# Performance work log

Measured on AMD Instinct MI355X. Metric: run time of the kernel, lower is better.

The kernel has to match this reference:

```python
import jax, jax.numpy as jnp
import numpy as np

WINDOW = 32


def _dilate(mask, iters=5):
    # scipy binary_dilation with default cross structure, `iters` iterations
    m = mask.copy()
    for _ in range(iters):
        d = m.copy()
        d[1:, :] |= m[:-1, :]
        d[:-1, :] |= m[1:, :]
        d[:, 1:] |= m[:, :-1]
        d[:, :-1] |= m[:, 1:]
        m = d
    return m


def _label8(mask):
    # skimage measure.label, default 8-connectivity, via min-label propagation
    h, w = mask.shape
    lab = np.where(mask, np.arange(1, mask.size + 1, dtype=np.int64).reshape(h, w), 0)
    BIG = mask.size + 2
    while True:
        p = np.pad(np.where(mask, lab, BIG), 1, constant_values=BIG)
        m = np.full((h, w), BIG, dtype=np.int64)
        for dy in (-1, 0, 1):
            for dx in (-1, 0, 1):
                m = np.minimum(m, p[1 + dy:1 + dy + h, 1 + dx:1 + dx + w])
        new = np.where(mask, m, 0)
        if np.array_equal(new, lab):
            break
        lab = new
    u = np.unique(lab)
    out = np.searchsorted(u, lab)
    if u[0] != 0:
        out = out + 1
    return out


def _malis(seg_flat, e1, e2, costs, pos):
    # MALIS edge weights: Kruskal on descending affinities with union-find;
    # pos=True counts same-(nonzero)-label pairs merged by each edge,
    # pos=False counts cross-label pairs between labeled nodes.
    n = seg_flat.size
    parent = np.arange(n)
    cnt = [dict() for _ in range(n)]
    for i in range(n):
        s = int(seg_flat[i])
        if s != 0:
            cnt[i][s] = 1
    w = np.zeros(costs.shape[0], np.float32)

    def find(x):
        r = x
        while parent[r] != r:
            r = parent[r]
        while parent[x] != r:
            parent[x], x = r, parent[x]
        return r

    order = np.argsort(-costs, kind='stable')
    for ei in order:
        ra, rb = find(int(e1[ei])), find(int(e2[ei]))
        if ra == rb:
            continue
        ca, cb = cnt[ra], cnt[rb]
        small, large = (ca, cb) if len(ca) <= len(cb) else (cb, ca)
        same = 0
        for kk, v in small.items():
            same += v * large.get(kk, 0)
        if pos:
            w[ei] = same
        else:
            sa = sum(ca.values())
            sb = sum(cb.values())
            w[ei] = sa * sb - same
        parent[rb] = ra
        for kk, v in cb.items():
            ca[kk] = ca.get(kk, 0) + v
        cnt[rb] = None
    return w


def compute_malis_weights(pred_np, target_np):
    B, C, H, W = pred_np.shape
    wn_full = np.zeros(pred_np.shape, np.float32)
    wp_full = np.zeros(pred_np.shape, np.float32)
    win = WINDOW
    idx = np.arange(win * win).reshape(win, win)
    e1 = np.concatenate([idx[:, :-1].ravel(), idx[:-1, :].ravel()])
    e2 = np.concatenate([idx[:, 1:].ravel(), idx[1:, :].ravel()])
    for k in range(H // win):
        for j in range(W // win):
            p = pred_np[:, :, k * win:(k + 1) * win, j * win:(j + 1) * win]
            t = target_np[:, :, k * win:(k + 1) * win, j * win:(j + 1) * win]
            costs = np.concatenate([
                (p[:, :, :, :-1] + p[:, :, :, 1:]).reshape(B, -1),
                (p[:, :, :-1, :] + p[:, :, 1:, :]).reshape(B, -1)], axis=1).astype(np.float32)
            gtc = np.concatenate([
                (t[:, :, :, :-1] + t[:, :, :, 1:]).reshape(B, -1),
                (t[:, :, :-1, :] + t[:, :, 1:, :]).reshape(B, -1)], axis=1).astype(np.float32)
            costs_n = costs.copy()
            costs_p = costs.copy()
            costs_n[gtc > 20] = 20
            costs_p[gtc < 10] = 0
            gtc = np.minimum(gtc, 20)
            for i in range(B):
                sg = _label8(_dilate(t[i, 0] == 0, 5) == 0)
                en = _malis(sg.ravel(), e1, e2, costs_n[i], False)
                ep = _malis(sg.ravel(), e1, e2, costs_p[i], True)
                sn = en.sum()
                if sn > 0:
                    en = en / sn
                sp = ep.sum()
                if sp > 0:
                    ep = ep / sp
                en[gtc[i] >= 10] = 0
                ep[gtc[i] < 20] = 0
                for ew, out in ((en, wn_full), (ep, wp_full)):
                    wh, wv = np.split(ew, 2)
                    wh = wh.reshape(win, win - 1)
                    wv = wv.reshape(win - 1, win)
                    nodes = np.zeros((win, win), np.float32)
                    nodes[:, :-1] += wh
                    nodes[:, 1:] += wh
                    nodes[:-1, :] += wv
                    nodes[1:, :] += wv
                    out[i, 0, k * win:(k + 1) * win, j * win:(j + 1) * win] = nodes
    return wn_full, wp_full


def setup_inputs() -> dict:
    key = jax.random.key(0)
    k1, k2 = jax.random.split(key)
    pred = jax.random.uniform(k1, (2, 1, 256, 256), jnp.float32) * 20.0
    target = jax.random.randint(k2, (2, 1, 256, 256), 0, 26).astype(jnp.float32)
    return {"pred": pred, "target": target, "malis_lr": 1.0, "malis_lr_pos": 1.0}


def reference(pred, target, malis_lr, malis_lr_pos):
    # weights are computed from detached values (CPU graph algorithm), constants wrt autodiff
    wn, wp = compute_malis_weights(np.asarray(pred), np.asarray(target))
    wn = jnp.asarray(wn, jnp.float32)
    wp = jnp.asarray(wp, jnp.float32)
    loss = malis_lr * jnp.square(pred) * wn + malis_lr_pos * jnp.square(20.0 - pred) * wp
    return loss.sum()
```

## Files before the change

### kernel.cpp

```cpp
#include <hip/hip_runtime.h>
#include <cstdint>

#define NPIX  1024
#define NH    992
#define NEDGE 1984
#define NSORT 2048
#define NGRP  31
#define HFS   4300
#define POOLN (NPIX + 2*HFS)

typedef unsigned long long u64;
typedef unsigned int u32;

static __device__ __forceinline__ u64 packRoot(int sL,int off,int len,int cap){
    return (u64)(u32)(sL & 0x7FF) | ((u64)(u32)(off & 0x3FFF) << 11) |
           ((u64)(u32)(len & 0x7FF) << 25) | ((u64)(u32)(cap & 0x7FF) << 36);
}
#define R_SL(R)  ((int)((R) & 0x7FF))
#define R_OFF(R) ((int)(((R)>>11) & 0x3FFF))
#define R_LEN(R) ((int)(((R)>>25) & 0x7FF))
#define R_CAP(R) ((int)(((R)>>36) & 0x7FF))

static __device__ __forceinline__ int rdl(int v, int l){ return __builtin_amdgcn_readlane(v, l); }

static __device__ __forceinline__ u64 sxor64(u64 v, int m){
    u32 lo = (u32)__shfl_xor((int)(v & 0xFFFFFFFFull), m, 64);
    u32 hi = (u32)__shfl_xor((int)(v >> 32), m, 64);
    return ((u64)hi << 32) | lo;
}

#define CE(x, y, up) { u64 _a=(x), _b=(y); bool _lt=(_a<_b); \
    u64 _mn=_lt?_a:_b, _mx=_lt?_b:_a; (x)=(up)?_mn:_mx; (y)=(up)?_mx:_mn; }
#define CEX(x, xm, keepmin) { u64 _p=sxor64((x),(xm)); bool _lt=((x)<_p); \
    u64 _mn=_lt?(x):_p, _mx=_lt?_p:(x); (x)=(keepmin)?_mn:_mx; }

static __device__ __forceinline__ int wredi(int v){
    #pragma unroll
    for (int o = 32; o > 0; o >>= 1) v += __shfl_xor(v, o, 64);
    return v;
}
static __device__ __forceinline__ float wredf(float v){
    #pragma unroll
    for (int o = 32; o > 0; o >>= 1) v += __shfl_xor(v, o, 64);
    return v;
}

__global__ __launch_bounds__(128) void malis_kernel(
    const float* __restrict__ pred,
    const float* __restrict__ target,
    const float* __restrict__ lr_p,
    const float* __restrict__ lrp_p,
    float* __restrict__ out)
{
    const int tid  = threadIdx.x;
    const int lane = tid & 63;
    const int wv   = tid >> 6;
    const int bid  = blockIdx.x;
    const int bb   = bid >> 6;
    const int win  = bid & 63;
    const int wy   = win >> 3, wx = win & 7;
    const int base = bb * 65536 + (wy * 32) * 256 + wx * 32;

    __shared__ __align__(16) u32 Ks[2][NSORT];
    __shared__ u64   root[2][NPIX];
    __shared__ float predL[NPIX];
    __shared__ float costs[NEDGE];
    __shared__ u32   eab[NEDGE];
    __shared__ u32   poolS[2][POOLN];
    __shared__ u32   Q[2][NPIX];
    __shared__ float Qw[2][NPIX];
    __shared__ short seg[NPIX];
    __shared__ short par[2][NPIX];
    __shared__ short H[2][NPIX + 1];
    __shared__ unsigned char tgtL[NPIX];
    __shared__ unsigned char gtcL[NEDGE];
    __shared__ int   flags[2];

    unsigned char* mA    = (unsigned char*)poolS;
    unsigned char* mB    = mA + NPIX;
    short*         labId = (short*)(mA + 2 * NPIX);

    for (int i = tid; i < NPIX; i += 128) {
        int r = i >> 5, c = i & 31;
        float pv = pred[base + r * 256 + c];
        float tv = target[base + r * 256 + c];
        predL[i] = pv;
        tgtL[i]  = (unsigned char)tv;
        mA[i]    = (tv == 0.0f) ? 1 : 0;
    }
    if (tid == 0) flags[1] = 0;
    __syncthreads();

    unsigned char* srcm = mA;
    unsigned char* dstm = mB;
    for (int it = 0; it < 5; ++it) {
        for (int i = tid; i < NPIX; i += 128) {
            int r = i >> 5, c = i & 31;
            unsigned char v = srcm[i];
            if (r > 0)  v |= srcm[i - 32];
            if (r < 31) v |= srcm[i + 32];
            if (c > 0)  v |= srcm[i - 1];
            if (c < 31) v |= srcm[i + 1];
            dstm[i] = v;
        }
        __syncthreads();
        unsigned char* t2 = srcm; srcm = dstm; dstm = t2;
    }

    for (int i = tid; i < NPIX; i += 128)
        seg[i] = srcm[i] ? (short)-1 : (short)i;
    __syncthreads();

    for (;;) {
        if (tid == 0) flags[0] = 0;
        __syncthreads();
        bool any = false;
        for (int i = tid; i < NPIX; i += 128) {
            int cur = seg[i];
            if (cur < 0) continue;
            int r = i >> 5, c = i & 31;
            int m = cur;
            if (r > 0) {
                if (c > 0)  { int t = seg[i - 33]; if (t >= 0 && t < m) m = t; }
                { int t = seg[i - 32]; if (t >= 0 && t < m) m = t; }
                if (c < 31) { int t = seg[i - 31]; if (t >= 0 && t < m) m = t; }
            }
            if (c > 0)  { int t = seg[i - 1]; if (t >= 0 && t < m) m = t; }
            if (c < 31) { int t = seg[i + 1]; if (t >= 0 && t < m) m = t; }
            if (r < 31) {
                if (c > 0)  { int t = seg[i + 31]; if (t >= 0 && t < m) m = t; }
                { int t = seg[i + 32]; if (t >= 0 && t < m) m = t; }
                if (c < 31) { int t = seg[i + 33]; if (t >= 0 && t < m) m = t; }
            }
            #pragma unroll
            for (int t2 = 0; t2 < 6; ++t2) {
                int s2 = seg[m];
                if (s2 >= 0 && s2 < m) m = s2; else break;
            }
            if (m < cur) { seg[i] = (short)m; any = true; }
        }
        if (any) flags[0] = 1;
        __syncthreads();
        if (flags[0] == 0) break;
        __syncthreads();
    }

    for (int i = tid; i < NPIX; i += 128)
        if (seg[i] == (short)i) labId[i] = (short)atomicAdd(&flags[1], 1);
    __syncthreads();
    for (int i = tid; i < NPIX; i += 128) {
        short s2 = seg[i];
        seg[i] = (s2 < 0) ? (short)0 : (short)(labId[s2] + 1);
    }

    for (int e = tid; e < NEDGE; e += 128) {
        int a, b2;
        if (e < NH) { int r = e / 31, c = e - r * 31; a = r * 32 + c; b2 = a + 1; }
        else        { int q = e - NH; int r = q >> 5, c = q & 31; a = r * 32 + c; b2 = a + 32; }
        eab[e]   = (u32)a | ((u32)b2 << 16);
        costs[e] = predL[a] + predL[b2];
        gtcL[e]  = (unsigned char)(tgtL[a] + tgtL[b2]);
    }
    __syncthreads();

    const int ph = wv;
    u32*   Ks_   = Ks[ph];
    short* par_  = par[ph];
    u64*   root_ = root[ph];
    u32*   pool_ = poolS[ph];
    short* H_    = H[ph];
    u32*   Q_    = Q[ph];
    float* Qw_   = Qw[ph];
    u32*   claim_= (u32*)Qw[ph];

    u64 sk[32];
    #pragma unroll
    for (int r = 0; r < 32; ++r) {
        int e = lane * 32 + r;
        u64 kv = ~0ULL;
        if (e < NEDGE) {
            float cv = costs[e];
            int g = gtcL[e];
            if (ph == 0) { if (g > 20) cv = 20.0f; }
            else         { if (g < 10) cv = 0.0f; }
            kv = (((u64)(~__float_as_uint(cv))) << 32) | (u32)e;
        }
        sk[r] = kv;
    }
    #pragma unroll
    for (int kk2 = 2; kk2 <= 32; kk2 <<= 1) {
        #pragma unroll
        for (int j = kk2 >> 1; j > 0; j >>= 1) {
            #pragma unroll
            for (int r = 0; r < 32; ++r) {
                if ((r & j) == 0) {
                    bool up = (kk2 == 32) ? ((lane & 1) == 0) : ((r & kk2) == 0);
                    CE(sk[r], sk[r | j], up);
                }
            }
        }
    }
    #pragma unroll
    for (int kk2 = 64; kk2 <= 2048; kk2 <<= 1) {
        const bool up = ((lane & (kk2 >> 5)) == 0);
        #pragma unroll
        for (int j = kk2 >> 1; j >= 32; j >>= 1) {
            const int xm = j >> 5;
            const bool keepmin = (((lane & xm) == 0) == up);
            #pragma unroll
            for (int r = 0; r < 32; ++r) { CEX(sk[r], xm, keepmin); }
        }
        #pragma unroll
        for (int j = 16; j > 0; j >>= 1) {
            #pragma unroll
            for (int r = 0; r < 32; ++r) {
                if ((r & j) == 0) { CE(sk[r], sk[r | j], up); }
            }
        }
    }
    #pragma unroll
    for (int r = 0; r < 32; r += 4) {
        uint4 v4;
        v4.x = (u32)sk[r]; v4.y = (u32)sk[r+1]; v4.z = (u32)sk[r+2]; v4.w = (u32)sk[r+3];
        *(uint4*)&Ks_[lane * 32 + r] = v4;
    }

    for (int i = lane; i < NPIX; i += 64) {
        par_[i] = (short)i;
        short s2 = seg[i];
        if (s2) {
            root_[i] = packRoot(1, i, 1, 1);
            pool_[i] = ((u32)(unsigned short)s2 << 16) | 1u;
        } else {
            root_[i] = 0;
        }
        H_[i] = 0;
        claim_[i] = ~0u;
    }
    if (lane == 0) H_[NPIX] = 0;
    __builtin_amdgcn_wave_barrier();

    int qn = 0;
    const u64 ltm = (1ull << lane) - 1;
    for (int g2 = 0; g2 < NGRP; ++g2) {
        int myE = (int)Ks_[g2 * 64 + lane];
        u32 ab = eab[myE];
        int ra = (int)(ab & 0xFFFF);
        int rb = (int)(ab >> 16);
        for (;;) {
            int pa = par_[ra], pb = par_[rb];
            bool fa = (pa != ra), fb = (pb != rb);
            if (!fa && !fb) break;
            int ga = par_[pa], gb = par_[pb];
            if (fa) { par_[ra] = (short)ga; ra = ga; }
            if (fb) { par_[rb] = (short)gb; rb = gb; }
        }
        bool laA = (seg[ra] != 0);
        bool laB = (seg[rb] != 0);
        bool alive = (ra != rb);

        for (;;) {
            if (!__ballot(alive)) break;
            const bool av = alive;
            int mn = ra < rb ? ra : rb;
            int mx = ra < rb ? rb : ra;
            int winner = (laA == laB) ? mn : (laA ? ra : rb);
            int loser  = (laA == laB) ? mx : (laA ? rb : ra);
            bool wgt = laA && laB;
            if (av)        atomicMin(&claim_[loser],  (u32)lane);
            if (av && wgt) atomicMin(&claim_[winner], (u32)lane);
            bool sel = false;
            if (av) {
                u32 cl = claim_[loser];
                u32 cw = wgt ? claim_[winner] : (u32)lane;
                sel = (cl == (u32)lane) && (cw == (u32)lane);
            }
            u64 wm = __ballot(sel && wgt);
            if (sel && wgt) Q_[qn + __popcll(wm & ltm)] =
                (u32)myE | ((u32)mn << 11) | ((u32)mx << 21);
            qn += (int)__popcll(wm);
            if (sel) par_[loser] = (short)winner;
            if (av) { claim_[loser] = ~0u; if (wgt) claim_[winner] = ~0u; }
            if (av) {
                int x = ra;
                for (;;) { int p = par_[x]; if (p == x) break; int q2 = par_[p]; par_[x] = (short)q2; x = q2; }
                int y = rb;
                for (;;) { int p = par_[y]; if (p == y) break; int q2 = par_[p]; par_[y] = (short)q2; y = q2; }
                ra = x; rb = y;
                laA = (seg[ra] != 0);
                laB = (seg[rb] != 0);
                alive = !sel && (ra != rb);
            }
        }
        __builtin_amdgcn_wave_barrier();
    }

    u32 bump = NPIX;
    u32 halfEnd = NPIX + HFS;
    int curHalf = 0;

    auto do_gc = [&]() {
        u32 tgt = (curHalf == 0) ? (u32)(NPIX + HFS) : (u32)NPIX;
        u32 nb = tgt;
        for (int c = 0; c < 16; ++c) {
            int i0 = c * 64 + lane;
            bool live = (root_[i0] != 0);
            u64 rbm = __ballot(live);
            while (rbm) {
                int j = __ffsll(rbm) - 1; rbm &= rbm - 1;
                int r = c * 64 + j;
                u64 R = root_[r];
                int len = R_LEN(R);
                int off = R_OFF(R);
                for (int t = lane; t < len; t += 64) {
                    u32 v2 = pool_[off + t];
                    pool_[nb + t] = v2;
                }
                __builtin_amdgcn_wave_barrier();
                if (lane == 0) root_[r] = packRoot(R_SL(R), (int)nb, len, len);
                nb += (u32)len;
            }
        }
        bump = nb;
        halfEnd = tgt + HFS;
        curHalf ^= 1;
    };

    for (int q = 0; q < qn; ++q) {
        u32 rec = Q_[q];
        int me = (int)(rec & 0x7FF);
        int A  = (int)((rec >> 11) & 0x3FF);
        int B  = (int)((rec >> 21) & 0x3FF);
        int winner = A;
        int dead   = B;
        u64 RA = root_[A], RB = root_[B];
        int sLa = R_SL(RA), sLb = R_SL(RB);
        int lenA = R_LEN(RA), lenB = R_LEN(RB);
        if (bump + (u32)(lenA + lenB + 8) > halfEnd) {
            do_gc();
            RA = root_[A]; RB = root_[B];
            lenA = R_LEN(RA); lenB = R_LEN(RB);
        }
        int offA = R_OFF(RA), capA = R_CAP(RA);
        int offB = R_OFF(RB), capB = R_CAP(RB);
        int offS, lenS, offL, lenL, capL;
        if (lenA <= lenB) { offS = offA; lenS = lenA; offL = offB; lenL = lenB; capL = capB; }
        else              { offS = offB; lenS = lenB; offL = offA; lenL = lenA; capL = capA; }
        int same = 0, dOff, dLen, dCap;

        if (lenS + lenL <= 64) {
            u32 eL = (lane < lenL) ? pool_[offL + lane] : 0u;
            u32 eS = (lane < lenS) ? pool_[offS + lane] : 0u;
            dLen = lenL;
            for (int t = 0; t < lenS; ++t) {
                u32 xs = (u32)rdl((int)eS, t);
                bool match = (lane < lenL) && ((eL >> 16) == (xs >> 16));
                u64 mb = __ballot(match);
                if (mb) {
                    int ml = __ffsll(mb) - 1;
                    same += (int)(xs & 0xFFFF) * ((int)rdl((int)eL, ml) & 0xFFFF);
                    if (match) eL += (xs & 0xFFFF);
                } else {
                    if (lane == dLen) eL = xs;
                    dLen++;
                }
            }
            if (dLen <= capL) { dOff = offL; dCap = capL; }
            else { dOff = (int)bump; dCap = (dLen + 3) & ~3; bump += (u32)dCap; }
            if (lane < dLen) pool_[dOff + lane] = eL;
        } else {
            dOff = (int)bump;
            dCap = (lenL + lenS + 4) & ~3; bump += (u32)dCap;
            for (int j = lane; j < lenS; j += 64) {
                u32 es = pool_[offS + j];
                H_[es >> 16] = (short)(es & 0xFFFF);
            }
            __builtin_amdgcn_wave_barrier();
            int sp = 0;
            for (int j = lane; j < lenL; j += 64) {
                u32 el = pool_[offL + j];
                int h = (int)H_[el >> 16];
                sp += h * (int)(el & 0xFFFF);
                pool_[dOff + j] = el + (u32)h;
                if (h) H_[el >> 16] = 0;
            }
            same = wredi(sp);
            __builtin_amdgcn_wave_barrier();
            int baseU = 0;
            for (int j0 = 0; j0 < lenS; j0 += 64) {
                int j = j0 + lane;
                bool un = false; u32 es = 0;
                if (j < lenS) { es = pool_[offS + j]; un = (H_[es >> 16] != 0); }
                u64 ub = __ballot(un);
                if (un) {
                    int pos = __popcll(ub & ltm);
                    pool_[dOff + lenL + baseU + pos] = es;
                    H_[es >> 16] = 0;
                }
                baseU += __popcll(ub);
            }
            dLen = lenL + baseU;
        }
        if (lane == 0) {
            Qw_[q] = (float)(ph ? same : (sLa * sLb - same));
            root_[winner] = packRoot(sLa + sLb, dOff, dLen, dCap);
            root_[dead]   = 0;
        }
        __builtin_amdgcn_wave_barrier();
    }

    float s_loc = 0.0f;
    for (int q = lane; q < qn; q += 64) s_loc += Qw_[q];
    const float sn = wredf(s_loc);

    const float scale = ph ? lrp_p[0] : lr_p[0];
    float acc = 0.0f;
    for (int q = lane; q < qn; q += 64) {
        float wv2 = Qw_[q];
        if (wv2 == 0.0f) continue;
        if (sn > 0.0f) wv2 /= sn;
        int me = (int)(Q_[q] & 0x7FF);
        int g = gtcL[me];
        bool zero = ph ? (g < 20) : (g >= 10);
        if (zero) continue;
        u32 ab = eab[me];
        float pa = predL[ab & 0xFFFF], pb = predL[ab >> 16];
        float fa2, fb2;
        if (ph == 0) { fa2 = pa * pa; fb2 = pb * pb; }
        else { float qa = 20.0f - pa, qb = 20.0f - pb; fa2 = qa * qa; fb2 = qb * qb; }
        acc += scale * wv2 * (fa2 + fb2);
    }
    acc = wredf(acc);
    if (lane == 0) atomicAdd(out, acc);
}

__global__ void zero_out_kernel(float* o)
{
    if (threadIdx.x == 0 && blockIdx.x == 0) o[0] = 0.0f;
}

extern "C" void kernel_launch(void* const* d_in, const int* in_sizes, int n_in,
                              void* d_out, int out_size, void* d_ws, size_t ws_size,
                              hipStream_t stream)
{
    const float* pred   = (const float*)d_in[0];
    const float* target = (const float*)d_in[1];
    const float* lr     = (const float*)d_in[2];
    const float* lrp    = (const float*)d_in[3];
    float* out = (float*)d_out;

    zero_out_kernel<<<1, 64, 0, stream>>>(out);
    malis_kernel<<<128, 128, 0, stream>>>(pred, target, lr, lrp, out);
}
```

Baseline: 380.1 us.

## Pack label bit into parent array, compute edge endpoints, and use round-tagged claims

Drops the eab shared table and recomputes edge endpoints arithmetically. Stores the labeled flag in the top bit of the parent entries so the find loop returns labels without separate seg reads. Replaces claim resets with monotonically decreasing round tags and prefetches the next group's sorted edge index. The aim is fewer LDS accesses and stores in the serial union-find phase. The cost is a 10-bit root mask that must stay correct and tag space that shrinks with each round.

```diff
diff --git a/kernel.cpp b/kernel.cpp
--- a/kernel.cpp
+++ b/kernel.cpp
@@ -27,6 +27,11 @@
     u32 lo = (u32)__shfl_xor((int)(v & 0xFFFFFFFFull), m, 64);
     u32 hi = (u32)__shfl_xor((int)(v >> 32), m, 64);
     return ((u64)hi << 32) | lo;
+}
+
+static __device__ __forceinline__ void edgeAB(int e, int &a, int &b){
+    if (e < NH) { int r = (int)((unsigned)e / 31u); a = e + r; b = a + 1; }
+    else        { a = e - NH; b = a + 32; }
 }
 
 #define CE(x, y, up) { u64 _a=(x), _b=(y); bool _lt=(_a<_b); \
@@ -65,7 +70,6 @@
     __shared__ u64   root[2][NPIX];
     __shared__ float predL[NPIX];
     __shared__ float costs[NEDGE];
-    __shared__ u32   eab[NEDGE];
     __shared__ u32   poolS[2][POOLN];
     __shared__ u32   Q[2][NPIX];
     __shared__ float Qw[2][NPIX];
@@ -154,10 +158,7 @@
     }
 
     for (int e = tid; e < NEDGE; e += 128) {
-        int a, b2;
-        if (e < NH) { int r = e / 31, c = e - r * 31; a = r * 32 + c; b2 = a + 1; }
-        else        { int q = e - NH; int r = q >> 5, c = q & 31; a = r * 32 + c; b2 = a + 32; }
-        eab[e]   = (u32)a | ((u32)b2 << 16);
+        int a, b2; edgeAB(e, a, b2);
         costs[e] = predL[a] + predL[b2];
         gtcL[e]  = (unsigned char)(tgtL[a] + tgtL[b2]);
     }
@@ -226,8 +227,8 @@
     }
 
     for (int i = lane; i < NPIX; i += 64) {
-        par_[i] = (short)i;
         short s2 = seg[i];
+        par_[i] = (short)(i | (s2 ? 0x8000 : 0));
         if (s2) {
             root_[i] = packRoot(1, i, 1, 1);
             pool_[i] = ((u32)(unsigned short)s2 << 16) | 1u;
@@ -241,57 +242,67 @@
     __builtin_amdgcn_wave_barrier();
 
     int qn = 0;
+    u32 rnd = 1;
     const u64 ltm = (1ull << lane) - 1;
+    int curE = (int)Ks_[lane];
     for (int g2 = 0; g2 < NGRP; ++g2) {
-        int myE = (int)Ks_[g2 * 64 + lane];
-        u32 ab = eab[myE];
-        int ra = (int)(ab & 0xFFFF);
-        int rb = (int)(ab >> 16);
+        int nextE = (g2 + 1 < NGRP) ? (int)Ks_[(g2 + 1) * 64 + lane] : 0;
+        const int myE = curE;
+        int ea, eb2; edgeAB(myE, ea, eb2);
+        int ra = ea, rb = eb2;
+        int laA, laB;
         for (;;) {
-            int pa = par_[ra], pb = par_[rb];
+            int va = (int)(unsigned short)par_[ra];
+            int vb = (int)(unsigned short)par_[rb];
+            int pa = va & 0x3FF, pb = vb & 0x3FF;
             bool fa = (pa != ra), fb = (pb != rb);
-            if (!fa && !fb) break;
-            int ga = par_[pa], gb = par_[pb];
-            if (fa) { par_[ra] = (short)ga; ra = ga; }
-            if (fb) { par_[rb] = (short)gb; rb = gb; }
-        }
-        bool laA = (seg[ra] != 0);
-        bool laB = (seg[rb] != 0);
+            if (!fa && !fb) { laA = va >> 15; laB = vb >> 15; break; }
+            int ga = (int)(unsigned short)par_[pa];
+            int gb = (int)(unsigned short)par_[pb];
+            if (fa) { par_[ra] = (short)ga; ra = ga & 0x3FF; }
+            if (fb) { par_[rb] = (short)gb; rb = gb & 0x3FF; }
+        }
         bool alive = (ra != rb);
 
         for (;;) {
             if (!__ballot(alive)) break;
             const bool av = alive;
+            const u32 tag = ((0x03FFFFFFu - rnd) << 6) | (u32)lane;
+            ++rnd;
             int mn = ra < rb ? ra : rb;
             int mx = ra < rb ? rb : ra;
             int winner = (laA == laB) ? mn : (laA ? ra : rb);
             int loser  = (laA == laB) ? mx : (laA ? rb : ra);
-            bool wgt = laA && laB;
-            if (av)        atomicMin(&claim_[loser],  (u32)lane);
-            if (av && wgt) atomicMin(&claim_[winner], (u32)lane);
+            bool wgt = (laA & laB) != 0;
+            if (av)        atomicMin(&claim_[loser],  tag);
+            if (av && wgt) atomicMin(&claim_[winner], tag);
             bool sel = false;
             if (av) {
                 u32 cl = claim_[loser];
-                u32 cw = wgt ? claim_[winner] : (u32)lane;
-                sel = (cl == (u32)lane) && (cw == (u32)lane);
+                u32 cw = wgt ? claim_[winner] : tag;
+                sel = (cl == tag) && (cw == tag);
             }
             u64 wm = __ballot(sel && wgt);
             if (sel && wgt) Q_[qn + __popcll(wm & ltm)] =
                 (u32)myE | ((u32)mn << 11) | ((u32)mx << 21);
             qn += (int)__popcll(wm);
             if (sel) par_[loser] = (short)winner;
-            if (av) { claim_[loser] = ~0u; if (wgt) claim_[winner] = ~0u; }
             if (av) {
-                int x = ra;
-                for (;;) { int p = par_[x]; if (p == x) break; int q2 = par_[p]; par_[x] = (short)q2; x = q2; }
-                int y = rb;
-                for (;;) { int p = par_[y]; if (p == y) break; int q2 = par_[p]; par_[y] = (short)q2; y = q2; }
-                ra = x; rb = y;
-                laA = (seg[ra] != 0);
-                laB = (seg[rb] != 0);
+                for (;;) {
+                    int va = (int)(unsigned short)par_[ra];
+                    int vb = (int)(unsigned short)par_[rb];
+                    int pa = va & 0x3FF, pb = vb & 0x3FF;
+                    bool fa = (pa != ra), fb = (pb != rb);
+                    if (!fa && !fb) { laA = va >> 15; laB = vb >> 15; break; }
+                    int ga = (int)(unsigned short)par_[pa];
+                    int gb = (int)(unsigned short)par_[pb];
+                    if (fa) { par_[ra] = (short)ga; ra = ga & 0x3FF; }
+                    if (fb) { par_[rb] = (short)gb; rb = gb & 0x3FF; }
+                }
                 alive = !sel && (ra != rb);
             }
         }
+        curE = nextE;
         __builtin_amdgcn_wave_barrier();
     }
 
@@ -328,7 +339,6 @@
 
     for (int q = 0; q < qn; ++q) {
         u32 rec = Q_[q];
-        int me = (int)(rec & 0x7FF);
         int A  = (int)((rec >> 11) & 0x3FF);
         int B  = (int)((rec >> 21) & 0x3FF);
         int winner = A;
@@ -423,8 +433,8 @@
         int g = gtcL[me];
         bool zero = ph ? (g < 20) : (g >= 10);
         if (zero) continue;
-        u32 ab = eab[me];
-        float pa = predL[ab & 0xFFFF], pb = predL[ab >> 16];
+        int a2, b2; edgeAB(me, a2, b2);
+        float pa = predL[a2], pb = predL[b2];
         float fa2, fb2;
         if (ph == 0) { fa2 = pa * pa; fb2 = pb * pb; }
         else { float qa = 20.0f - pa, qb = 20.0f - pb; fa2 = qa * qa; fb2 = qb * qb; }
```

Result: no change. 374.8 us (-1.4%).
